# Performance work log

Hardware: AMD Instinct MI355X
Metric: run time of the kernel (lower is better)

The kernel has to match this reference:

```python
import jax, jax.numpy as jnp
import numpy as np

SHAPES = ((496, 432), (248, 216), (124, 108))
NS = (40000, 20000, 8000)
T = 32
B = 4
EPS = 1e-3


def _bn(x, g, b, m, v):
    return (x - m) * (g / jnp.sqrt(v + EPS)) + b


def _vfe_scale(voxels, num_pts, w1, p1, w2, p2):
    # voxels: (N, T, 4); num_pts: (N,)
    Tp = voxels.shape[1]
    n = num_pts.astype(voxels.dtype)[:, None, None]
    m3 = voxels[:, :, :3].sum(axis=1, keepdims=True) / n
    m2 = voxels[:, :, :2].sum(axis=1, keepdims=True) / n
    feat = jnp.concatenate([voxels[:, :, :4], voxels[:, :, :3] - m3, voxels[:, :, :2] - m2], axis=-1)  # (N,T,9)
    mask = (jnp.arange(Tp)[None, :] < num_pts[:, None]).astype(voxels.dtype)[:, :, None]
    x = feat
    for w, (g, b_, rm, rv) in ((w1, p1), (w2, p2)):
        h = jax.nn.relu(_bn(jnp.einsum('ntc,cd->ntd', x, w), g, b_, rm, rv))  # (N,T,64)
        gmax = h.max(axis=1, keepdims=True)  # global max includes padded rows, as in torch source
        x = jnp.concatenate([h, jnp.broadcast_to(gmax, h.shape)], axis=-1) * mask  # (N,T,128)
    return x.max(axis=1)[:, :64]  # (N,64)


def _scatter_bev(vf, coords, h, w, batch_size):
    b = coords[:, 0]
    y = jnp.clip(coords[:, 2], 0, h - 1)
    x = jnp.clip(coords[:, 3], 0, w - 1)
    grid = jnp.zeros((batch_size, vf.shape[1], h, w), vf.dtype)
    return grid.at[b, :, y, x].set(vf)


def _fusion(x, w, g, b, m, v):
    y = jax.lax.conv_general_dilated(x, w, (1, 1), ((1, 1), (1, 1)),
                                     dimension_numbers=('NCHW', 'OIHW', 'NCHW'))
    y = _bn(y, g[None, :, None, None], b[None, :, None, None], m[None, :, None, None], v[None, :, None, None])
    return jax.nn.relu(y)


def setup_inputs() -> dict:
    key = jax.random.key(0)
    ks = jax.random.split(key, 32)
    inp = {}
    for s in range(3):
        h, w = SHAPES[s]
        inp[f'voxels_{s}'] = jax.random.normal(ks[s], (NS[s], T, 4), dtype=jnp.float32)
        inp[f'num_pts_{s}'] = jax.random.randint(ks[3 + s], (NS[s],), 1, T + 1, dtype=jnp.int32)
        b = jax.random.randint(ks[6 + s], (NS[s],), 0, B, dtype=jnp.int32)
        z = jnp.zeros((NS[s],), jnp.int32)
        y = jax.random.randint(ks[9 + s], (NS[s],), 0, h, dtype=jnp.int32)
        x = jax.random.randint(ks[12 + s], (NS[s],), 0, w, dtype=jnp.int32)
        inp[f'coords_{s}'] = jnp.stack([b, z, y, x], axis=1)
    # VFE params (stacked across the 3 scales; identical shapes per scale)
    inp['w1'] = jax.random.normal(ks[15], (3, 9, 64), dtype=jnp.float32) * 0.1
    inp['g1'] = jnp.ones((3, 64), jnp.float32) + 0.1 * jax.random.normal(ks[16], (3, 64))
    inp['b1'] = 0.05 * jax.random.normal(ks[17], (3, 64))
    inp['rm1'] = 0.05 * jax.random.normal(ks[18], (3, 64))
    inp['rv1'] = 0.5 + jnp.abs(jax.random.normal(ks[19], (3, 64)))
    inp['w2'] = jax.random.normal(ks[20], (3, 128, 64), dtype=jnp.float32) * 0.05
    inp['g2'] = jnp.ones((3, 64), jnp.float32) + 0.1 * jax.random.normal(ks[21], (3, 64))
    inp['b2'] = 0.05 * jax.random.normal(ks[22], (3, 64))
    inp['rm2'] = 0.05 * jax.random.normal(ks[23], (3, 64))
    inp['rv2'] = 0.5 + jnp.abs(jax.random.normal(ks[24], (3, 64)))
    # Fusion convs (2): Conv2d(128,64,3) + BN
    inp['fw'] = jax.random.normal(ks[25], (2, 64, 128, 3, 3), dtype=jnp.float32) * 0.03
    inp['fg'] = jnp.ones((2, 64), jnp.float32) + 0.1 * jax.random.normal(ks[26], (2, 64))
    inp['fb'] = 0.05 * jax.random.normal(ks[27], (2, 64))
    inp['fm'] = 0.05 * jax.random.normal(ks[28], (2, 64))
    inp['fv'] = 0.5 + jnp.abs(jax.random.normal(ks[29], (2, 64)))
    inp['batch_size'] = B
    return inp


def reference(voxels_0, voxels_1, voxels_2,
              w1, g1, b1, rm1, rv1, w2, g2, b2, rm2, rv2,
              fw, fg, fb, fm, fv,
              num_pts_0, num_pts_1, num_pts_2,
              coords_0, coords_1, coords_2, batch_size):
    voxels = (voxels_0, voxels_1, voxels_2)
    num_pts = (num_pts_0, num_pts_1, num_pts_2)
    coords = (coords_0, coords_1, coords_2)
    sf = []
    for s in range(3):
        vf = _vfe_scale(voxels[s], num_pts[s],
                        w1[s], (g1[s], b1[s], rm1[s], rv1[s]),
                        w2[s], (g2[s], b2[s], rm2[s], rv2[s]))
        h, w = SHAPES[s]
        sf.append(_scatter_bev(vf, coords[s], h, w, batch_size))
    # bottom-up fusion: scale2 -> scale1 -> scale0
    up = jax.image.resize(sf[2], sf[1].shape[:2] + SHAPES[1], method='bilinear')
    fused_1 = _fusion(jnp.concatenate([sf[1], up], axis=1), fw[1], fg[1], fb[1], fm[1], fv[1])
    up = jax.image.resize(fused_1, fused_1.shape[:2] + SHAPES[0], method='bilinear')
    fused_0 = _fusion(jnp.concatenate([sf[0], up], axis=1), fw[0], fg[0], fb[0], fm[0], fv[0])
    return fused_0  # spatial_features_2d: (B, 64, 496, 432)
```

## Files before the change

kernel.cpp:

```cpp
#include <hip/hip_runtime.h>

typedef unsigned short u16;
typedef short bf16x8 __attribute__((ext_vector_type(8)));
typedef float f32x4 __attribute__((ext_vector_type(4)));

#define EPSV 1e-3f

__device__ __forceinline__ float bf2f(u16 u) {
  union { unsigned int i; float f; } x; x.i = ((unsigned int)u) << 16; return x.f;
}
__device__ __forceinline__ u16 f2bf(float f) {
  union { float f; unsigned int i; } x; x.f = f;
  unsigned int r = x.i + 0x7fffu + ((x.i >> 16) & 1u);
  return (u16)(r >> 16);
}

#define WAVE_FENCE() do { __builtin_amdgcn_s_waitcnt(0); __builtin_amdgcn_wave_barrier(); } while (0)

__global__ void twt_kernel(const float* __restrict__ fw, u16* __restrict__ fwT) {
  int i = blockIdx.x * blockDim.x + threadIdx.x;
  if (i >= 2 * 9 * 64 * 128) return;
  int ci = i & 127;
  int r = i >> 7;
  int co = r & 63; r >>= 6;
  int kyx = r % 9;
  int set = r / 9;
  fwT[i] = f2bf(fw[(((set * 64 + co) * 128 + ci) * 9) + kyx]);
}

__global__ __launch_bounds__(256, 2) void vfe_mfma_kernel(
    const float* __restrict__ vox, const int* __restrict__ npts,
    const float* __restrict__ w1, const float* __restrict__ g1, const float* __restrict__ b1,
    const float* __restrict__ rm1, const float* __restrict__ rv1,
    const float* __restrict__ w2, const float* __restrict__ g2, const float* __restrict__ b2,
    const float* __restrict__ rm2, const float* __restrict__ rv2,
    float* __restrict__ vf, int N)
{
  struct PerWave {
    u16 X[32 * 72];
    u16 F[32 * 40];
    u16 G[64];
  };
  __shared__ __align__(16) union {
    struct { u16 W1T[64 * 40]; u16 W2T[64 * 136]; } w;
    PerWave r[4];
  } lds;

  const int tid = threadIdx.x;
  const int lane = tid & 63;
  const int wv = tid >> 6;
  const int m16 = lane & 15;
  const int q = lane >> 4;

  for (int i = tid; i < 64 * 40; i += 256) {
    int c = i / 40, k = i % 40;
    lds.w.W1T[i] = f2bf(k < 9 ? w1[k * 64 + c] : 0.f);
  }
  for (int i = tid; i < 64 * 136; i += 256) {
    int c = i / 136, j = i % 136;
    lds.w.W2T[i] = f2bf(j < 128 ? w2[j * 64 + c] : 0.f);
  }
  __syncthreads();

  bf16x8 bW1[4], bLo[4][2], bHi[4][2];
  float sc1[4], sh1[4], sc2[4], sh2[4];
#pragma unroll
  for (int nf = 0; nf < 4; ++nf) {
    int c = nf * 16 + m16;
    bW1[nf] = *(const bf16x8*)&lds.w.W1T[c * 40 + q * 8];
#pragma unroll
    for (int ks = 0; ks < 2; ++ks) {
      bLo[nf][ks] = *(const bf16x8*)&lds.w.W2T[c * 136 + ks * 32 + q * 8];
      bHi[nf][ks] = *(const bf16x8*)&lds.w.W2T[c * 136 + 64 + ks * 32 + q * 8];
    }
    float s1 = g1[c] * rsqrtf(rv1[c] + EPSV);
    sc1[nf] = s1; sh1[nf] = b1[c] - rm1[c] * s1;
    float s2 = g2[c] * rsqrtf(rv2[c] + EPSV);
    sc2[nf] = s2; sh2[nf] = b2[c] - rm2[c] * s2;
  }
  __syncthreads();

  u16* X = lds.r[wv].X;
  u16* F = lds.r[wv].F;
  u16* G = lds.r[wv].G;
  for (int i = lane; i < 640; i += 64) ((unsigned int*)F)[i] = 0u;

  const int wgid = blockIdx.x * 4 + wv;
  const int wstride = gridDim.x * 4;

  for (int v = wgid; v < N; v += wstride) {
    const int n = npts[v];
    float px = 0.f, py = 0.f, pz = 0.f, pw = 0.f;
    if (lane < 32) {
      float4 u = *(const float4*)(vox + ((size_t)v * 32 + lane) * 4);
      px = u.x; py = u.y; pz = u.z; pw = u.w;
    }
    float sx = px, sy = py, sz = pz;
#pragma unroll
    for (int off = 32; off >= 1; off >>= 1) {
      sx += __shfl_xor(sx, off);
      sy += __shfl_xor(sy, off);
      sz += __shfl_xor(sz, off);
    }
    float nf_ = (float)n;
    float mx = sx / nf_, my = sy / nf_, mz = sz / nf_;
    if (lane < 32) {
      float dx = px - mx, dy = py - my, dz = pz - mz;
      bf16x8 r0, r1;
      r0[0] = (short)f2bf(px); r0[1] = (short)f2bf(py);
      r0[2] = (short)f2bf(pz); r0[3] = (short)f2bf(pw);
      r0[4] = (short)f2bf(dx); r0[5] = (short)f2bf(dy);
      r0[6] = (short)f2bf(dz); r0[7] = (short)f2bf(dx);
      r1 = (bf16x8){0, 0, 0, 0, 0, 0, 0, 0};
      r1[0] = (short)f2bf(dy);
      *(bf16x8*)&F[lane * 40 + 0] = r0;
      *(bf16x8*)&F[lane * 40 + 8] = r1;
    }
    WAVE_FENCE();

    bf16x8 a1[2];
    a1[0] = *(const bf16x8*)&F[m16 * 40 + q * 8];
    a1[1] = *(const bf16x8*)&F[(16 + m16) * 40 + q * 8];
    f32x4 acc1[2][4];
#pragma unroll
    for (int mf = 0; mf < 2; ++mf)
#pragma unroll
      for (int nf = 0; nf < 4; ++nf) {
        acc1[mf][nf] = (f32x4){0.f, 0.f, 0.f, 0.f};
        acc1[mf][nf] = __builtin_amdgcn_mfma_f32_16x16x32_bf16(a1[mf], bW1[nf], acc1[mf][nf], 0, 0, 0);
      }

    float gmx[4] = {0.f, 0.f, 0.f, 0.f};
#pragma unroll
    for (int mf = 0; mf < 2; ++mf)
#pragma unroll
      for (int nf = 0; nf < 4; ++nf)
#pragma unroll
        for (int r = 0; r < 4; ++r) {
          float h = fmaxf(acc1[mf][nf][r] * sc1[nf] + sh1[nf], 0.f);
          gmx[nf] = fmaxf(gmx[nf], h);
          int t = mf * 16 + q * 4 + r;
          X[t * 72 + nf * 16 + m16] = f2bf(h);
        }
#pragma unroll
    for (int nf = 0; nf < 4; ++nf) {
      gmx[nf] = fmaxf(gmx[nf], __shfl_xor(gmx[nf], 16));
      gmx[nf] = fmaxf(gmx[nf], __shfl_xor(gmx[nf], 32));
    }
    if (q == 0) {
#pragma unroll
      for (int nf = 0; nf < 4; ++nf) G[nf * 16 + m16] = f2bf(gmx[nf]);
    }
    WAVE_FENCE();

    f32x4 ga[4];
#pragma unroll
    for (int nf = 0; nf < 4; ++nf) ga[nf] = (f32x4){0.f, 0.f, 0.f, 0.f};
#pragma unroll
    for (int ks = 0; ks < 2; ++ks) {
      bf16x8 ag = (bf16x8){0, 0, 0, 0, 0, 0, 0, 0};
      if (m16 == 0) ag = *(const bf16x8*)&G[ks * 32 + q * 8];
#pragma unroll
      for (int nf = 0; nf < 4; ++nf)
        ga[nf] = __builtin_amdgcn_mfma_f32_16x16x32_bf16(ag, bHi[nf][ks], ga[nf], 0, 0, 0);
    }
    float gt[4];
#pragma unroll
    for (int nf = 0; nf < 4; ++nf) {
      float s = ga[nf][0] + ga[nf][1] + ga[nf][2] + ga[nf][3];
      s += __shfl_xor(s, 16);
      s += __shfl_xor(s, 32);
      gt[nf] = s;
    }

    f32x4 acc2[2][4];
#pragma unroll
    for (int mf = 0; mf < 2; ++mf)
#pragma unroll
      for (int nf = 0; nf < 4; ++nf)
        acc2[mf][nf] = (f32x4){gt[nf], gt[nf], gt[nf], gt[nf]};
#pragma unroll
    for (int ks = 0; ks < 2; ++ks) {
      bf16x8 a2[2];
      a2[0] = *(const bf16x8*)&X[m16 * 72 + ks * 32 + q * 8];
      a2[1] = *(const bf16x8*)&X[(16 + m16) * 72 + ks * 32 + q * 8];
#pragma unroll
      for (int mf = 0; mf < 2; ++mf)
#pragma unroll
        for (int nf = 0; nf < 4; ++nf)
          acc2[mf][nf] = __builtin_amdgcn_mfma_f32_16x16x32_bf16(a2[mf], bLo[nf][ks], acc2[mf][nf], 0, 0, 0);
    }

    float vm[4] = {0.f, 0.f, 0.f, 0.f};
#pragma unroll
    for (int mf = 0; mf < 2; ++mf)
#pragma unroll
      for (int nf = 0; nf < 4; ++nf)
#pragma unroll
        for (int r = 0; r < 4; ++r) {
          int t = mf * 16 + q * 4 + r;
          float h2 = fmaxf(acc2[mf][nf][r] * sc2[nf] + sh2[nf], 0.f);
          if (t < n) vm[nf] = fmaxf(vm[nf], h2);
        }
#pragma unroll
    for (int nf = 0; nf < 4; ++nf) {
      vm[nf] = fmaxf(vm[nf], __shfl_xor(vm[nf], 16));
      vm[nf] = fmaxf(vm[nf], __shfl_xor(vm[nf], 32));
    }
    float outv = (q == 0) ? vm[0] : (q == 1) ? vm[1] : (q == 2) ? vm[2] : vm[3];
    vf[(size_t)v * 64 + q * 16 + m16] = outv;
    __builtin_amdgcn_wave_barrier();
  }
}

__global__ void winner_kernel(const int* __restrict__ coords, int* __restrict__ win,
                              int N, int H, int W) {
  int v = blockIdx.x * blockDim.x + threadIdx.x;
  if (v >= N) return;
  int b = coords[v * 4 + 0];
  int y = min(max(coords[v * 4 + 2], 0), H - 1);
  int x = min(max(coords[v * 4 + 3], 0), W - 1);
  atomicMax(&win[(b * H + y) * W + x], v);
}

__global__ void fill_kernel(const int* __restrict__ win, const float* __restrict__ vf,
                            u16* __restrict__ dst, int cells, int cstride) {
  int i = blockIdx.x * blockDim.x + threadIdx.x;
  if (i >= cells * 8) return;
  int cell = i >> 3, c8 = (i & 7) * 8;
  int wv = win[cell];
  bf16x8 o = (bf16x8){0, 0, 0, 0, 0, 0, 0, 0};
  if (wv >= 0) {
    const float* p = vf + (size_t)wv * 64 + c8;
    float4 v0 = *(const float4*)p;
    float4 v1 = *(const float4*)(p + 4);
    o[0] = (short)f2bf(v0.x); o[1] = (short)f2bf(v0.y);
    o[2] = (short)f2bf(v0.z); o[3] = (short)f2bf(v0.w);
    o[4] = (short)f2bf(v1.x); o[5] = (short)f2bf(v1.y);
    o[6] = (short)f2bf(v1.z); o[7] = (short)f2bf(v1.w);
  }
  *(bf16x8*)&dst[(size_t)cell * cstride + c8] = o;
}

__global__ void upsample_kernel(const u16* __restrict__ src, u16* __restrict__ dst,
                                int Hc, int Wc, int dstride, int doff, int total8) {
  int i = blockIdx.x * blockDim.x + threadIdx.x;
  if (i >= total8) return;
  int c8 = (i & 7) * 8;
  int px = i >> 3;
  int W2 = Wc * 2, H2 = Hc * 2;
  int x = px % W2; int t = px / W2; int y = t % H2; int n = t / H2;
  int ky = y >> 1, kx = x >> 1;
  int ya, yb, xa, xb; float wya, wxa;
  if ((y & 1) == 0) { ya = ky > 0 ? ky - 1 : 0; yb = ky; wya = 0.25f; }
  else              { ya = ky; yb = (ky + 1 < Hc) ? ky + 1 : Hc - 1; wya = 0.75f; }
  if ((x & 1) == 0) { xa = kx > 0 ? kx - 1 : 0; xb = kx; wxa = 0.25f; }
  else              { xa = kx; xb = (kx + 1 < Wc) ? kx + 1 : Wc - 1; wxa = 0.75f; }
  float wyb = 1.f - wya, wxb = 1.f - wxa;
  const u16* sp = src + c8;
  bf16x8 vaa = *(const bf16x8*)&sp[((size_t)(n * Hc + ya) * Wc + xa) * 64];
  bf16x8 vab = *(const bf16x8*)&sp[((size_t)(n * Hc + ya) * Wc + xb) * 64];
  bf16x8 vba = *(const bf16x8*)&sp[((size_t)(n * Hc + yb) * Wc + xa) * 64];
  bf16x8 vbb = *(const bf16x8*)&sp[((size_t)(n * Hc + yb) * Wc + xb) * 64];
  bf16x8 o;
#pragma unroll
  for (int j = 0; j < 8; ++j) {
    float v = wya * (wxa * bf2f((u16)vaa[j]) + wxb * bf2f((u16)vab[j])) +
              wyb * (wxa * bf2f((u16)vba[j]) + wxb * bf2f((u16)vbb[j]));
    o[j] = (short)f2bf(v);
  }
  *(bf16x8*)&dst[(size_t)px * dstride + doff + c8] = o;
}

template<int H, int W, bool NCHW_OUT>
__global__ __launch_bounds__(256, 2) void conv_kernel(
    const u16* __restrict__ in, const u16* __restrict__ wT,
    const float* __restrict__ fg, const float* __restrict__ fb,
    const float* __restrict__ fm, const float* __restrict__ fv,
    void* __restrict__ outv)
{
  constexpr int XT = 32, YT = 8;
  constexpr int XTILES = (W + XT - 1) / XT;
  constexpr int CIP = 72;
  constexpr int NPX = 10 * 34;
  __shared__ __align__(16) union {
    struct { u16 A[NPX * CIP]; u16 B[2][64 * CIP]; } s;
    float T[4 * 64 * 33];
  } lds;

  const int tid = threadIdx.x;
  const int lane = tid & 63;
  const int wv = tid >> 6;
  const int m16 = lane & 15;
  const int q = lane >> 4;

  int bid = blockIdx.x;
  const int xt = bid % XTILES; bid /= XTILES;
  const int yt = bid % (H / YT);
  const int n = bid / (H / YT);
  const int x0 = xt * XT, y0 = yt * YT;

  float sc[4], sh[4];
#pragma unroll
  for (int nf = 0; nf < 4; ++nf) {
    int co = nf * 16 + m16;
    float s = fg[co] * rsqrtf(fv[co] + EPSV);
    sc[nf] = s;
    sh[nf] = fb[co] - fm[co] * s;
  }

  f32x4 acc[4][4];
#pragma unroll
  for (int mf = 0; mf < 4; ++mf)
#pragma unroll
    for (int nf = 0; nf < 4; ++nf)
      acc[mf][nf] = (f32x4){0.f, 0.f, 0.f, 0.f};

  for (int hf = 0; hf < 2; ++hf) {
    {
      const int cis = (tid & 7) * 8;
#pragma unroll
      for (int it = 0; it < 11; ++it) {
        int p = (tid >> 3) + it * 32;
        if (p < NPX) {
          int r = p / 34, xx = p - r * 34;
          int gy = y0 - 1 + r, gx = x0 - 1 + xx;
          uint4 v = make_uint4(0, 0, 0, 0);
          if (gy >= 0 && gy < H && gx >= 0 && gx < W)
            v = *(const uint4*)(in + ((size_t)((n * H + gy) * W + gx) * 128 + hf * 64 + cis));
          *(uint4*)&lds.s.A[p * CIP + cis] = v;
        }
      }
    }
    {
#pragma unroll
      for (int it = 0; it < 2; ++it) {
        int e8 = (it * 256 + tid) * 8;
        int co = e8 >> 6, ci = e8 & 63;
        uint4 v = *(const uint4*)(wT + (co * 128 + hf * 64 + ci));
        *(uint4*)&lds.s.B[0][co * CIP + ci] = v;
      }
    }
    __syncthreads();

    for (int kyx = 0; kyx < 9; ++kyx) {
      if (kyx < 8) {
#pragma unroll
        for (int it = 0; it < 2; ++it) {
          int e8 = (it * 256 + tid) * 8;
          int co = e8 >> 6, ci = e8 & 63;
          uint4 v = *(const uint4*)(wT + ((kyx + 1) * 8192 + co * 128 + hf * 64 + ci));
          *(uint4*)&lds.s.B[(kyx + 1) & 1][co * CIP + ci] = v;
        }
      }
      const int ky = kyx / 3, kx = kyx - ky * 3;
      const u16* Bb = lds.s.B[kyx & 1];
#pragma unroll
      for (int cc = 0; cc < 2; ++cc) {
        bf16x8 a[4], b[4];
#pragma unroll
        for (int mf = 0; mf < 4; ++mf) {
          int p = (wv * 2 + (mf >> 1) + ky) * 34 + (mf & 1) * 16 + m16 + kx;
          a[mf] = *(const bf16x8*)&lds.s.A[p * CIP + cc * 32 + q * 8];
        }
#pragma unroll
        for (int nf = 0; nf < 4; ++nf)
          b[nf] = *(const bf16x8*)&Bb[(nf * 16 + m16) * CIP + cc * 32 + q * 8];
#pragma unroll
        for (int mf = 0; mf < 4; ++mf)
#pragma unroll
          for (int nf = 0; nf < 4; ++nf)
            acc[mf][nf] = __builtin_amdgcn_mfma_f32_16x16x32_bf16(a[mf], b[nf], acc[mf][nf], 0, 0, 0);
      }
      __syncthreads();
    }
  }

  if (!NCHW_OUT) {
    u16* out = (u16*)outv;
#pragma unroll
    for (int mf = 0; mf < 4; ++mf) {
      int y = y0 + wv * 2 + (mf >> 1);
#pragma unroll
      for (int nf = 0; nf < 4; ++nf)
#pragma unroll
        for (int r = 0; r < 4; ++r) {
          int px = (mf & 1) * 16 + q * 4 + r;
          int x = x0 + px;
          if (x < W) {
            int co = nf * 16 + m16;
            float v = fmaxf(acc[mf][nf][r] * sc[nf] + sh[nf], 0.f);
            out[((size_t)(n * H + y) * W + x) * 64 + co] = f2bf(v);
          }
        }
    }
  } else {
    float* out = (float*)outv;
    float* T = &lds.T[wv * 64 * 33];
#pragma unroll
    for (int yr = 0; yr < 2; ++yr) {
#pragma unroll
      for (int xc = 0; xc < 2; ++xc)
#pragma unroll
        for (int nf = 0; nf < 4; ++nf)
#pragma unroll
          for (int r = 0; r < 4; ++r) {
            int px = xc * 16 + q * 4 + r;
            int co = nf * 16 + m16;
            T[co * 33 + px] = fmaxf(acc[yr * 2 + xc][nf][r] * sc[nf] + sh[nf], 0.f);
          }
      WAVE_FENCE();
      const int px = lane & 31, co2 = lane >> 5;
      const int y = y0 + wv * 2 + yr;
      int x = x0 + px;
#pragma unroll 4
      for (int it = 0; it < 32; ++it) {
        int co = it * 2 + co2;
        float v = T[co * 33 + px];
        if (x < W) out[((size_t)(n * 64 + co) * H + y) * W + x] = v;
      }
      WAVE_FENCE();
    }
  }
}

extern "C" void kernel_launch(void* const* d_in, const int* in_sizes, int n_in,
                              void* d_out, int out_size, void* d_ws, size_t ws_size,
                              hipStream_t stream) {
  int I_vox[3], I_np[3], I_co[3];
  int I_w1, I_g1, I_b1, I_rm1, I_rv1, I_w2, I_g2, I_b2, I_rm2, I_rv2;
  int I_fw, I_fg, I_fb, I_fm, I_fv;
  if (in_sizes[1] == 40000) {
    I_vox[0] = 0; I_np[0] = 1; I_co[0] = 2;
    I_vox[1] = 3; I_np[1] = 4; I_co[1] = 5;
    I_vox[2] = 6; I_np[2] = 7; I_co[2] = 8;
    I_w1 = 9; I_g1 = 10; I_b1 = 11; I_rm1 = 12; I_rv1 = 13;
    I_w2 = 14; I_g2 = 15; I_b2 = 16; I_rm2 = 17; I_rv2 = 18;
    I_fw = 19; I_fg = 20; I_fb = 21; I_fm = 22; I_fv = 23;
  } else {
    I_vox[0] = 0; I_vox[1] = 1; I_vox[2] = 2;
    I_w1 = 3; I_g1 = 4; I_b1 = 5; I_rm1 = 6; I_rv1 = 7;
    I_w2 = 8; I_g2 = 9; I_b2 = 10; I_rm2 = 11; I_rv2 = 12;
    I_fw = 13; I_fg = 14; I_fb = 15; I_fm = 16; I_fv = 17;
    I_np[0] = 18; I_np[1] = 19; I_np[2] = 20;
    I_co[0] = 21; I_co[1] = 22; I_co[2] = 23;
  }

  const int HS[3] = {496, 248, 124};
  const int WS[3] = {432, 216, 108};
  int Nv[3];
  for (int s = 0; s < 3; ++s) Nv[s] = in_sizes[I_np[s]];

  char* wsp = (char*)d_ws;
  size_t off = 0;
  auto take = [&](size_t bytes) -> void* {
    void* p = wsp + off;
    off = (off + bytes + 255) & ~(size_t)255;
    return p;
  };
  float* vf[3]; int* win[3];
  for (int s = 0; s < 3; ++s) vf[s] = (float*)take((size_t)Nv[s] * 64 * 4);
  int cells[3];
  for (int s = 0; s < 3; ++s) {
    cells[s] = 4 * HS[s] * WS[s];
    win[s] = (int*)take((size_t)cells[s] * 4);
  }
  u16* buf0 = (u16*)take((size_t)cells[0] * 128 * 2);
  u16* buf1 = (u16*)take((size_t)cells[1] * 128 * 2);
  u16* g2b  = (u16*)take((size_t)cells[2] * 64 * 2);
  u16* fus1 = (u16*)take((size_t)cells[1] * 64 * 2);
  u16* fwT  = (u16*)take((size_t)2 * 9 * 64 * 128 * 2);

  const float* W1 = (const float*)d_in[I_w1];
  const float* G1 = (const float*)d_in[I_g1];
  const float* B1 = (const float*)d_in[I_b1];
  const float* RM1 = (const float*)d_in[I_rm1];
  const float* RV1 = (const float*)d_in[I_rv1];
  const float* W2 = (const float*)d_in[I_w2];
  const float* G2 = (const float*)d_in[I_g2];
  const float* B2 = (const float*)d_in[I_b2];
  const float* RM2 = (const float*)d_in[I_rm2];
  const float* RV2 = (const float*)d_in[I_rv2];
  const float* FW = (const float*)d_in[I_fw];
  const float* FG = (const float*)d_in[I_fg];
  const float* FB = (const float*)d_in[I_fb];
  const float* FM = (const float*)d_in[I_fm];
  const float* FV = (const float*)d_in[I_fv];

  for (int s = 0; s < 3; ++s)
    hipMemsetAsync(win[s], 0xFF, (size_t)cells[s] * 4, stream);

  twt_kernel<<<(2 * 9 * 64 * 128 + 255) / 256, 256, 0, stream>>>(FW, fwT);

  for (int s = 0; s < 3; ++s) {
    int blocks = (Nv[s] + 3) / 4;
    if (blocks > 1024) blocks = 1024;
    vfe_mfma_kernel<<<blocks, 256, 0, stream>>>(
        (const float*)d_in[I_vox[s]], (const int*)d_in[I_np[s]],
        W1 + s * 9 * 64, G1 + s * 64, B1 + s * 64, RM1 + s * 64, RV1 + s * 64,
        W2 + s * 128 * 64, G2 + s * 64, B2 + s * 64, RM2 + s * 64, RV2 + s * 64,
        vf[s], Nv[s]);
  }
  for (int s = 0; s < 3; ++s) {
    winner_kernel<<<(Nv[s] + 255) / 256, 256, 0, stream>>>(
        (const int*)d_in[I_co[s]], win[s], Nv[s], HS[s], WS[s]);
  }
  fill_kernel<<<(cells[0] * 8 + 255) / 256, 256, 0, stream>>>(win[0], vf[0], buf0, cells[0], 128);
  fill_kernel<<<(cells[1] * 8 + 255) / 256, 256, 0, stream>>>(win[1], vf[1], buf1, cells[1], 128);
  fill_kernel<<<(cells[2] * 8 + 255) / 256, 256, 0, stream>>>(win[2], vf[2], g2b, cells[2], 64);

  {
    int total8 = cells[1] * 8;
    upsample_kernel<<<(total8 + 255) / 256, 256, 0, stream>>>(g2b, buf1, 124, 108, 128, 64, total8);
  }
  conv_kernel<248, 216, false><<<4 * (248 / 8) * 7, 256, 0, stream>>>(
      buf1, fwT + 9 * 64 * 128, FG + 64, FB + 64, FM + 64, FV + 64, fus1);
  {
    int total8 = cells[0] * 8;
    upsample_kernel<<<(total8 + 255) / 256, 256, 0, stream>>>(fus1, buf0, 248, 216, 128, 64, total8);
  }
  conv_kernel<496, 432, true><<<4 * (496 / 8) * 14, 256, 0, stream>>>(
      buf0, fwT, FG, FB, FM, FV, (float*)d_out);
}
```

Before: 775.8 us.

## Fuse scatter-fill and bilinear upsample into conv input loads; merge per-scale launches

The conv kernel now builds its input halo tile directly: the first 64 channels come from the winner map and voxel features (converted to bf16 on the fly), and the second 64 come from bilinear interpolation of the coarser map. This removes the large intermediate 128-channel BEV buffers, their fill and upsample kernels, and the associated write/read traffic. The three VFE launches, three winner launches and three memsets are also merged into single launches. In exchange, each conv tile does gather loads and interpolation arithmetic, including recomputation for halo pixels, so the input-loading phase becomes more irregular.

```diff
diff --git a/kernel.cpp b/kernel.cpp
--- a/kernel.cpp
+++ b/kernel.cpp
@@ -28,13 +28,15 @@
   fwT[i] = f2bf(fw[(((set * 64 + co) * 128 + ci) * 9) + kyx]);
 }
 
-__global__ __launch_bounds__(256, 2) void vfe_mfma_kernel(
-    const float* __restrict__ vox, const int* __restrict__ npts,
-    const float* __restrict__ w1, const float* __restrict__ g1, const float* __restrict__ b1,
-    const float* __restrict__ rm1, const float* __restrict__ rv1,
-    const float* __restrict__ w2, const float* __restrict__ g2, const float* __restrict__ b2,
-    const float* __restrict__ rm2, const float* __restrict__ rv2,
-    float* __restrict__ vf, int N)
+__global__ __launch_bounds__(256, 2) void vfe_all_kernel(
+    const float* __restrict__ vox0, const float* __restrict__ vox1, const float* __restrict__ vox2,
+    const int* __restrict__ np0, const int* __restrict__ np1, const int* __restrict__ np2,
+    const float* __restrict__ W1g, const float* __restrict__ G1, const float* __restrict__ B1,
+    const float* __restrict__ RM1, const float* __restrict__ RV1,
+    const float* __restrict__ W2g, const float* __restrict__ G2, const float* __restrict__ B2,
+    const float* __restrict__ RM2, const float* __restrict__ RV2,
+    float* __restrict__ vf0, float* __restrict__ vf1, float* __restrict__ vf2,
+    int nb0, int nb1, int nb2, int N0, int N1, int N2)
 {
   struct PerWave {
     u16 X[32 * 72];
@@ -52,6 +54,19 @@
   const int m16 = lane & 15;
   const int q = lane >> 4;
 
+  int bid = blockIdx.x;
+  int s, lbid, nb, N;
+  const float* vox; const int* npts; float* vf;
+  if (bid < nb0)            { s = 0; lbid = bid;             nb = nb0; vox = vox0; npts = np0; vf = vf0; N = N0; }
+  else if (bid < nb0 + nb1) { s = 1; lbid = bid - nb0;       nb = nb1; vox = vox1; npts = np1; vf = vf1; N = N1; }
+  else                      { s = 2; lbid = bid - nb0 - nb1; nb = nb2; vox = vox2; npts = np2; vf = vf2; N = N2; }
+  const float* w1 = W1g + s * 9 * 64;
+  const float* g1 = G1 + s * 64;  const float* b1 = B1 + s * 64;
+  const float* rm1 = RM1 + s * 64; const float* rv1 = RV1 + s * 64;
+  const float* w2 = W2g + s * 128 * 64;
+  const float* g2 = G2 + s * 64;  const float* b2 = B2 + s * 64;
+  const float* rm2 = RM2 + s * 64; const float* rv2 = RV2 + s * 64;
+
   for (int i = tid; i < 64 * 40; i += 256) {
     int c = i / 40, k = i % 40;
     lds.w.W1T[i] = f2bf(k < 9 ? w1[k * 64 + c] : 0.f);
@@ -85,8 +100,8 @@
   u16* G = lds.r[wv].G;
   for (int i = lane; i < 640; i += 64) ((unsigned int*)F)[i] = 0u;
 
-  const int wgid = blockIdx.x * 4 + wv;
-  const int wstride = gridDim.x * 4;
+  const int wgid = lbid * 4 + wv;
+  const int wstride = nb * 4;
 
   for (int v = wgid; v < N; v += wstride) {
     const int n = npts[v];
@@ -167,10 +182,10 @@
     float gt[4];
 #pragma unroll
     for (int nf = 0; nf < 4; ++nf) {
-      float s = ga[nf][0] + ga[nf][1] + ga[nf][2] + ga[nf][3];
-      s += __shfl_xor(s, 16);
-      s += __shfl_xor(s, 32);
-      gt[nf] = s;
+      float s_ = ga[nf][0] + ga[nf][1] + ga[nf][2] + ga[nf][3];
+      s_ += __shfl_xor(s_, 16);
+      s_ += __shfl_xor(s_, 32);
+      gt[nf] = s_;
     }
 
     f32x4 acc2[2][4];
@@ -213,14 +228,20 @@
   }
 }
 
-__global__ void winner_kernel(const int* __restrict__ coords, int* __restrict__ win,
-                              int N, int H, int W) {
-  int v = blockIdx.x * blockDim.x + threadIdx.x;
-  if (v >= N) return;
-  int b = coords[v * 4 + 0];
-  int y = min(max(coords[v * 4 + 2], 0), H - 1);
-  int x = min(max(coords[v * 4 + 3], 0), W - 1);
-  atomicMax(&win[(b * H + y) * W + x], v);
+__global__ void winner_all_kernel(
+    const int* __restrict__ c0, const int* __restrict__ c1, const int* __restrict__ c2,
+    int* __restrict__ w0, int* __restrict__ w1, int* __restrict__ w2,
+    int N0, int N1, int N2) {
+  int i = blockIdx.x * blockDim.x + threadIdx.x;
+  const int* co; int* wn; int H, W, v;
+  if (i < N0) { co = c0; wn = w0; H = 496; W = 432; v = i; }
+  else if (i < N0 + N1) { co = c1; wn = w1; H = 248; W = 216; v = i - N0; }
+  else if (i < N0 + N1 + N2) { co = c2; wn = w2; H = 124; W = 108; v = i - N0 - N1; }
+  else return;
+  int b = co[v * 4 + 0];
+  int y = min(max(co[v * 4 + 2], 0), H - 1);
+  int x = min(max(co[v * 4 + 3], 0), W - 1);
+  atomicMax(&wn[(b * H + y) * W + x], v);
 }
 
 __global__ void fill_kernel(const int* __restrict__ win, const float* __restrict__ vf,
@@ -242,14 +263,8 @@
   *(bf16x8*)&dst[(size_t)cell * cstride + c8] = o;
 }
 
-__global__ void upsample_kernel(const u16* __restrict__ src, u16* __restrict__ dst,
-                                int Hc, int Wc, int dstride, int doff, int total8) {
-  int i = blockIdx.x * blockDim.x + threadIdx.x;
-  if (i >= total8) return;
-  int c8 = (i & 7) * 8;
-  int px = i >> 3;
-  int W2 = Wc * 2, H2 = Hc * 2;
-  int x = px % W2; int t = px / W2; int y = t % H2; int n = t / H2;
+template<int Hc, int Wc>
+__device__ __forceinline__ bf16x8 bilerp8(const u16* __restrict__ src, int n, int y, int x, int cis) {
   int ky = y >> 1, kx = x >> 1;
   int ya, yb, xa, xb; float wya, wxa;
   if ((y & 1) == 0) { ya = ky > 0 ? ky - 1 : 0; yb = ky; wya = 0.25f; }
@@ -257,7 +272,7 @@
   if ((x & 1) == 0) { xa = kx > 0 ? kx - 1 : 0; xb = kx; wxa = 0.25f; }
   else              { xa = kx; xb = (kx + 1 < Wc) ? kx + 1 : Wc - 1; wxa = 0.75f; }
   float wyb = 1.f - wya, wxb = 1.f - wxa;
-  const u16* sp = src + c8;
+  const u16* sp = src + cis;
   bf16x8 vaa = *(const bf16x8*)&sp[((size_t)(n * Hc + ya) * Wc + xa) * 64];
   bf16x8 vab = *(const bf16x8*)&sp[((size_t)(n * Hc + ya) * Wc + xb) * 64];
   bf16x8 vba = *(const bf16x8*)&sp[((size_t)(n * Hc + yb) * Wc + xa) * 64];
@@ -269,12 +284,13 @@
               wyb * (wxa * bf2f((u16)vba[j]) + wxb * bf2f((u16)vbb[j]));
     o[j] = (short)f2bf(v);
   }
-  *(bf16x8*)&dst[(size_t)px * dstride + doff + c8] = o;
+  return o;
 }
 
 template<int H, int W, bool NCHW_OUT>
 __global__ __launch_bounds__(256, 2) void conv_kernel(
-    const u16* __restrict__ in, const u16* __restrict__ wT,
+    const int* __restrict__ win, const float* __restrict__ vfsrc,
+    const u16* __restrict__ upsrc, const u16* __restrict__ wT,
     const float* __restrict__ fg, const float* __restrict__ fb,
     const float* __restrict__ fm, const float* __restrict__ fv,
     void* __restrict__ outv)
@@ -325,10 +341,24 @@
         if (p < NPX) {
           int r = p / 34, xx = p - r * 34;
           int gy = y0 - 1 + r, gx = x0 - 1 + xx;
-          uint4 v = make_uint4(0, 0, 0, 0);
-          if (gy >= 0 && gy < H && gx >= 0 && gx < W)
-            v = *(const uint4*)(in + ((size_t)((n * H + gy) * W + gx) * 128 + hf * 64 + cis));
-          *(uint4*)&lds.s.A[p * CIP + cis] = v;
+          bf16x8 o = (bf16x8){0, 0, 0, 0, 0, 0, 0, 0};
+          if (gy >= 0 && gy < H && gx >= 0 && gx < W) {
+            if (hf == 0) {
+              int wvx = win[(n * H + gy) * W + gx];
+              if (wvx >= 0) {
+                const float* pv = vfsrc + (size_t)wvx * 64 + cis;
+                float4 v0 = *(const float4*)pv;
+                float4 v1 = *(const float4*)(pv + 4);
+                o[0] = (short)f2bf(v0.x); o[1] = (short)f2bf(v0.y);
+                o[2] = (short)f2bf(v0.z); o[3] = (short)f2bf(v0.w);
+                o[4] = (short)f2bf(v1.x); o[5] = (short)f2bf(v1.y);
+                o[6] = (short)f2bf(v1.z); o[7] = (short)f2bf(v1.w);
+              }
+            } else {
+              o = bilerp8<H / 2, W / 2>(upsrc, n, gy, gx, cis);
+            }
+          }
+          *(bf16x8*)&lds.s.A[p * CIP + cis] = o;
         }
       }
     }
@@ -458,15 +488,14 @@
     off = (off + bytes + 255) & ~(size_t)255;
     return p;
   };
-  float* vf[3]; int* win[3];
+  float* vf[3];
   for (int s = 0; s < 3; ++s) vf[s] = (float*)take((size_t)Nv[s] * 64 * 4);
   int cells[3];
-  for (int s = 0; s < 3; ++s) {
-    cells[s] = 4 * HS[s] * WS[s];
-    win[s] = (int*)take((size_t)cells[s] * 4);
-  }
-  u16* buf0 = (u16*)take((size_t)cells[0] * 128 * 2);
-  u16* buf1 = (u16*)take((size_t)cells[1] * 128 * 2);
+  for (int s = 0; s < 3; ++s) cells[s] = 4 * HS[s] * WS[s];
+  size_t winbytes = ((size_t)cells[0] + cells[1] + cells[2]) * 4;
+  int* win0 = (int*)take(winbytes);
+  int* win1 = win0 + cells[0];
+  int* win2 = win1 + cells[1];
   u16* g2b  = (u16*)take((size_t)cells[2] * 64 * 2);
   u16* fus1 = (u16*)take((size_t)cells[1] * 64 * 2);
   u16* fwT  = (u16*)take((size_t)2 * 9 * 64 * 128 * 2);
@@ -487,38 +516,31 @@
   const float* FM = (const float*)d_in[I_fm];
   const float* FV = (const float*)d_in[I_fv];
 
-  for (int s = 0; s < 3; ++s)
-    hipMemsetAsync(win[s], 0xFF, (size_t)cells[s] * 4, stream);
+  hipMemsetAsync(win0, 0xFF, winbytes, stream);
 
   twt_kernel<<<(2 * 9 * 64 * 128 + 255) / 256, 256, 0, stream>>>(FW, fwT);
 
+  int nb[3];
   for (int s = 0; s < 3; ++s) {
-    int blocks = (Nv[s] + 3) / 4;
-    if (blocks > 1024) blocks = 1024;
-    vfe_mfma_kernel<<<blocks, 256, 0, stream>>>(
-        (const float*)d_in[I_vox[s]], (const int*)d_in[I_np[s]],
-        W1 + s * 9 * 64, G1 + s * 64, B1 + s * 64, RM1 + s * 64, RV1 + s * 64,
-        W2 + s * 128 * 64, G2 + s * 64, B2 + s * 64, RM2 + s * 64, RV2 + s * 64,
-        vf[s], Nv[s]);
-  }
-  for (int s = 0; s < 3; ++s) {
-    winner_kernel<<<(Nv[s] + 255) / 256, 256, 0, stream>>>(
-        (const int*)d_in[I_co[s]], win[s], Nv[s], HS[s], WS[s]);
-  }
-  fill_kernel<<<(cells[0] * 8 + 255) / 256, 256, 0, stream>>>(win[0], vf[0], buf0, cells[0], 128);
-  fill_kernel<<<(cells[1] * 8 + 255) / 256, 256, 0, stream>>>(win[1], vf[1], buf1, cells[1], 128);
-  fill_kernel<<<(cells[2] * 8 + 255) / 256, 256, 0, stream>>>(win[2], vf[2], g2b, cells[2], 64);
-
-  {
-    int total8 = cells[1] * 8;
-    upsample_kernel<<<(total8 + 255) / 256, 256, 0, stream>>>(g2b, buf1, 124, 108, 128, 64, total8);
-  }
+    nb[s] = (Nv[s] + 3) / 4;
+    if (nb[s] > 1024) nb[s] = 1024;
+  }
+  vfe_all_kernel<<<nb[0] + nb[1] + nb[2], 256, 0, stream>>>(
+      (const float*)d_in[I_vox[0]], (const float*)d_in[I_vox[1]], (const float*)d_in[I_vox[2]],
+      (const int*)d_in[I_np[0]], (const int*)d_in[I_np[1]], (const int*)d_in[I_np[2]],
+      W1, G1, B1, RM1, RV1, W2, G2, B2, RM2, RV2,
+      vf[0], vf[1], vf[2],
+      nb[0], nb[1], nb[2], Nv[0], Nv[1], Nv[2]);
+
+  winner_all_kernel<<<(Nv[0] + Nv[1] + Nv[2] + 255) / 256, 256, 0, stream>>>(
+      (const int*)d_in[I_co[0]], (const int*)d_in[I_co[1]], (const int*)d_in[I_co[2]],
+      win0, win1, win2, Nv[0], Nv[1], Nv[2]);
+
+  fill_kernel<<<(cells[2] * 8 + 255) / 256, 256, 0, stream>>>(win2, vf[2], g2b, cells[2], 64);
+
   conv_kernel<248, 216, false><<<4 * (248 / 8) * 7, 256, 0, stream>>>(
-      buf1, fwT + 9 * 64 * 128, FG + 64, FB + 64, FM + 64, FV + 64, fus1);
-  {
-    int total8 = cells[0] * 8;
-    upsample_kernel<<<(total8 + 255) / 256, 256, 0, stream>>>(fus1, buf0, 248, 216, 128, 64, total8);
-  }
+      win1, vf[1], g2b, fwT + 9 * 64 * 128, FG + 64, FB + 64, FM + 64, FV + 64, fus1);
+
   conv_kernel<496, 432, true><<<4 * (496 / 8) * 14, 256, 0, stream>>>(
-      buf0, fwT, FG, FB, FM, FV, (float*)d_out);
-}
+      win0, vf[0], fus1, fwT, FG, FB, FM, FV, (float*)d_out);
+}
```

Result: no change. 785.9 us (+1.3%).
